# Kernel tuning notes

Measured on AMD Instinct MI355X. Metric: run time of the kernel, lower is better.

Reference implementation:

```python
import jax, jax.numpy as jnp
import numpy as np

N = 20000      # num nodes
E = 200000     # num edges (no self loops; GATConv adds them)
ND = 128       # node_feature_dim
ED = 64        # edge_feature_dim
H = 256        # hidden_dim (= GAT out_channels per head, concat=False)
HEADS = 4
L = 3          # num_gnn_layers


def setup_inputs() -> dict:
    key = jax.random.key(0)
    ks = jax.random.split(key, 24)
    rng = np.random.default_rng(0)
    src = rng.integers(0, N, size=E)
    dst = (src + 1 + rng.integers(0, N - 1, size=E)) % N  # guaranteed no self loops
    edge_index = jnp.asarray(np.stack([src, dst]), dtype=jnp.int32)
    s = 0.05
    inp = {
        'node_features': jax.random.normal(ks[0], (N, ND), jnp.float32),
        'edge_attr': jax.random.normal(ks[1], (E, ED), jnp.float32),
        'enc_w': jax.random.normal(ks[2], (ND, H), jnp.float32) * s,
        'enc_b': jnp.zeros((H,), jnp.float32),
        'edge_enc_w': jax.random.normal(ks[3], (L, ED, H), jnp.float32) * s,
        'edge_enc_b': jnp.zeros((L, H), jnp.float32),
        'gat_w': jax.random.normal(ks[4], (L, H, HEADS * H), jnp.float32) * s,
        'att_src': jax.random.normal(ks[5], (L, HEADS, H), jnp.float32) * s,
        'att_dst': jax.random.normal(ks[6], (L, HEADS, H), jnp.float32) * s,
        'att_edge': jax.random.normal(ks[7], (L, HEADS, H), jnp.float32) * s,
        'lin_edge_w': jax.random.normal(ks[8], (L, 1, HEADS * H), jnp.float32) * s,
        'gat_b': jnp.zeros((L, H), jnp.float32),
        'ln_g': jnp.ones((L, H), jnp.float32),
        'ln_b': jnp.zeros((L, H), jnp.float32),
        'head_w1': jax.random.normal(ks[9], (4, H, H // 2), jnp.float32) * s,
        'head_b1': jnp.zeros((4, H // 2), jnp.float32),
        'head_w2': jax.random.normal(ks[10], (4, H // 2, 1), jnp.float32) * s,
        'head_b2': jnp.zeros((4, 1), jnp.float32),
        'edge_index': edge_index,
    }
    return inp


def _layernorm(x, g, b, eps=1e-5):
    mu = x.mean(-1, keepdims=True)
    v = ((x - mu) ** 2).mean(-1, keepdims=True)
    return g * (x - mu) / jnp.sqrt(v + eps) + b


def _gat_layer(x, src, dst, ew_full, w, a_s_vec, a_d_vec, a_e_vec, lew, bias):
    # x: [N,H]; GATConv(heads=4, concat=False) with scalar edge feature (edge_dim=1)
    xp = (x @ w).reshape(N, HEADS, H)                       # [N,HEADS,H]
    a_s = (xp * a_s_vec).sum(-1)                            # [N,HEADS]
    a_d = (xp * a_d_vec).sum(-1)                            # [N,HEADS]
    ef = (ew_full[:, None] @ lew).reshape(-1, HEADS, H)     # [Etot,HEADS,H]
    a_e = (ef * a_e_vec).sum(-1)                            # [Etot,HEADS]
    logits = jax.nn.leaky_relu(a_s[src] + a_d[dst] + a_e, 0.2)
    m = jax.ops.segment_max(logits, dst, num_segments=N)    # segment softmax over dst
    p = jnp.exp(logits - m[dst])
    ssum = jax.ops.segment_sum(p, dst, num_segments=N)
    alpha = p / ssum[dst]                                   # [Etot,HEADS]
    out = jax.ops.segment_sum(alpha[:, :, None] * xp[src], dst, num_segments=N)
    return out.mean(1) + bias                               # concat=False -> mean over heads


def reference(node_features, edge_attr, enc_w, enc_b, edge_enc_w, edge_enc_b,
              gat_w, att_src, att_dst, att_edge, lin_edge_w, gat_b,
              ln_g, ln_b, head_w1, head_b1, head_w2, head_b2, edge_index):
    src0, dst0 = edge_index[0], edge_index[1]
    loop = jnp.arange(N, dtype=edge_index.dtype)
    src = jnp.concatenate([src0, loop])   # self loops appended (GATConv add_self_loops)
    dst = jnp.concatenate([dst0, loop])
    deg = jax.ops.segment_sum(jnp.ones((E,), node_features.dtype), dst0, num_segments=N)

    x = jax.nn.relu(node_features @ enc_w + enc_b)          # node encoder (dropout: eval)
    for l in range(L):
        ew = (edge_attr @ edge_enc_w[l] + edge_enc_b[l]).mean(-1)  # [E] scalar edge weight
        loop_w = jax.ops.segment_sum(ew, dst0, num_segments=N) / jnp.maximum(deg, 1.0)
        ew_full = jnp.concatenate([ew, loop_w])             # fill_value='mean' for self loops
        h = _gat_layer(x, src, dst, ew_full, gat_w[l], att_src[l], att_dst[l],
                       att_edge[l], lin_edge_w[l], gat_b[l])
        h = _layernorm(h, ln_g[l], ln_b[l])
        x = jax.nn.relu(x + h)
    emb = x                                                 # [N,H]

    # 4 prediction heads vectorized: k in {attrition, engagement, collaboration, anomaly}
    hmid = jax.nn.relu(jnp.einsum('nd,kdh->knh', emb, head_w1) + head_b1[:, None, :])
    o = jnp.einsum('knh,kho->kno', hmid, head_w2) + head_b2[:, None, :]  # [4,N,1]
    attrition = jax.nn.sigmoid(o[0])
    engagement = o[1]
    collaboration = o[2]
    anomaly = jax.nn.sigmoid(o[3])
    return (attrition, engagement, collaboration, anomaly, emb)
```

## Files before the change

kernel.cpp:

```cpp
#include <hip/hip_runtime.h>
#include <math.h>

#define N_NODES 20000
#define N_EDGES 200000
#define NDIM 128
#define EDIM 64
#define HDIM 256
#define HEADS 4
#define NH 1024
#define NLAYERS 3
#define SCAN_NBLK ((N_NODES + 255) / 256)

typedef __attribute__((ext_vector_type(8))) short short8;
typedef __attribute__((ext_vector_type(4))) float floatx4;

__device__ __forceinline__ float b2f(unsigned short u) {
    union { unsigned u; float f; } c; c.u = ((unsigned)u) << 16; return c.f;
}
__device__ __forceinline__ float b2f_lo(unsigned u) {
    union { unsigned u; float f; } c; c.u = u << 16; return c.f;
}
__device__ __forceinline__ float b2f_hi(unsigned u) {
    union { unsigned u; float f; } c; c.u = u & 0xffff0000u; return c.f;
}
__device__ __forceinline__ unsigned short f2b(float f) {
    union { float f; unsigned u; } c; c.f = f;
    unsigned u = c.u;
    return (unsigned short)((u + 0x7FFFu + ((u >> 16) & 1u)) >> 16);
}
__device__ __forceinline__ float lrelu(float v) { return v > 0.f ? v : 0.2f * v; }

__global__ void hist_kernel(const int* __restrict__ dst0, int* __restrict__ cnt) {
    int e = blockIdx.x * 256 + threadIdx.x;
    if (e < N_EDGES) atomicAdd(&cnt[dst0[e]], 1);
}

__global__ void scan_local(const int* __restrict__ cnt, int* __restrict__ row_ptr,
                           int* __restrict__ bsum) {
    __shared__ int wsum[4];
    int tid = threadIdx.x, lane = tid & 63, wid = tid >> 6;
    int n = blockIdx.x * 256 + tid;
    int v = (n < N_NODES) ? cnt[n] : 0;
    int s = v;
    #pragma unroll
    for (int off = 1; off < 64; off <<= 1) {
        int t = __shfl_up(s, off, 64);
        if (lane >= off) s += t;
    }
    if (lane == 63) wsum[wid] = s;
    __syncthreads();
    int woff = 0;
    #pragma unroll
    for (int w = 0; w < 4; w++) if (w < wid) woff += wsum[w];
    if (n < N_NODES) row_ptr[n] = woff + s - v;
    if (tid == 255) bsum[blockIdx.x] = woff + s;
}

__global__ void scan_bsums(int* __restrict__ bsum, int* __restrict__ boff) {
    __shared__ int wsum[2];
    int tid = threadIdx.x, lane = tid & 63, wid = tid >> 6;
    int v = (tid < SCAN_NBLK) ? bsum[tid] : 0;
    int s = v;
    #pragma unroll
    for (int off = 1; off < 64; off <<= 1) {
        int t = __shfl_up(s, off, 64);
        if (lane >= off) s += t;
    }
    if (lane == 63) wsum[wid] = s;
    __syncthreads();
    int woff = (wid == 1) ? wsum[0] : 0;
    if (tid < SCAN_NBLK) boff[tid] = woff + s - v;
    if (tid == SCAN_NBLK - 1) boff[SCAN_NBLK] = woff + s;
}

__global__ void scan_add(int* __restrict__ row_ptr, const int* __restrict__ boff) {
    int n = blockIdx.x * 256 + threadIdx.x;
    if (n < N_NODES) row_ptr[n] += boff[blockIdx.x];
    if (n == 0) row_ptr[N_NODES] = boff[SCAN_NBLK];
}

__global__ __launch_bounds__(256) void fill_ew(const int* __restrict__ src0,
                                               const int* __restrict__ dst0,
                                               const float* __restrict__ edge_attr,
                                               const float* __restrict__ wmean3,
                                               const float* __restrict__ scal3,
                                               const int* __restrict__ row_ptr,
                                               int* __restrict__ fillc,
                                               int* __restrict__ srcCSR,
                                               float* __restrict__ ewCSR4) {
    int e = blockIdx.x * 256 + threadIdx.x;
    if (e >= N_EDGES) return;
    int d = dst0[e];
    int p = atomicAdd(&fillc[d], 1);
    int pos = row_ptr[d] + p;
    srcCSR[pos] = src0[e];
    const float* row = edge_attr + (size_t)e * EDIM;
    float s0 = 0.f, s1 = 0.f, s2 = 0.f;
    #pragma unroll
    for (int dd = 0; dd < EDIM; dd += 4) {
        float4 a  = *(const float4*)(row + dd);
        float4 w0 = *(const float4*)(wmean3 + dd);
        float4 w1 = *(const float4*)(wmean3 + 64 + dd);
        float4 w2 = *(const float4*)(wmean3 + 128 + dd);
        s0 += a.x * w0.x + a.y * w0.y + a.z * w0.z + a.w * w0.w;
        s1 += a.x * w1.x + a.y * w1.y + a.z * w1.z + a.w * w1.w;
        s2 += a.x * w2.x + a.y * w2.y + a.z * w2.z + a.w * w2.w;
    }
    *(float4*)(ewCSR4 + (size_t)pos * 4) =
        make_float4(s0 + scal3[4], s1 + scal3[12], s2 + scal3[20], 0.f);
}

__global__ void transpose_bf(const float* __restrict__ in, unsigned short* __restrict__ out,
                             int K, int Nn, size_t in_bs, size_t out_bs) {
    in += blockIdx.z * in_bs;
    out += blockIdx.z * out_bs;
    __shared__ float sh[32][33];
    int tx = threadIdx.x, ty = threadIdx.y;
    int kb = blockIdx.y * 32, nb = blockIdx.x * 32;
    #pragma unroll
    for (int i = 0; i < 32; i += 8)
        sh[ty + i][tx] = in[(size_t)(kb + ty + i) * Nn + nb + tx];
    __syncthreads();
    #pragma unroll
    for (int i = 0; i < 32; i += 8)
        out[(size_t)(nb + ty + i) * K + kb + tx] = f2b(sh[tx][ty + i]);
}

__global__ void gat_w_prep(const float* __restrict__ in, unsigned short* __restrict__ out) {
    int z = blockIdx.z, l = z >> 2, h = z & 3;
    __shared__ float sh[32][33];
    int tx = threadIdx.x, ty = threadIdx.y;
    int kb = blockIdx.y * 32, db = blockIdx.x * 32;
    const float* src = in + (size_t)l * HDIM * NH + (size_t)h * HDIM;
    unsigned short* dst = out + (size_t)l * HDIM * NH + (size_t)h * HDIM;
    #pragma unroll
    for (int i = 0; i < 32; i += 8)
        sh[ty + i][tx] = src[(size_t)(kb + ty + i) * NH + db + tx];
    __syncthreads();
    #pragma unroll
    for (int i = 0; i < 32; i += 8)
        dst[(size_t)(db + ty + i) * NH + kb + tx] = f2b(0.25f * sh[tx][ty + i]);
}

__global__ void ws_prep(const float* __restrict__ gat_w, const float* __restrict__ att_src,
                        const float* __restrict__ att_dst,
                        float* __restrict__ ws_s, float* __restrict__ ws_d) {
    int l = blockIdx.x >> 2, h = blockIdx.x & 3;
    int k = threadIdx.x;
    const float* wrow = gat_w + (size_t)l * HDIM * NH + (size_t)k * NH + h * HDIM;
    const float* as = att_src + (size_t)l * NH + h * HDIM;
    const float* ad = att_dst + (size_t)l * NH + h * HDIM;
    float s1 = 0.f, s2 = 0.f;
    for (int d = 0; d < HDIM; d += 4) {
        float4 w4 = *(const float4*)(wrow + d);
        float4 a4 = *(const float4*)(as + d);
        float4 b4 = *(const float4*)(ad + d);
        s1 += w4.x * a4.x + w4.y * a4.y + w4.z * a4.z + w4.w * a4.w;
        s2 += w4.x * b4.x + w4.y * b4.y + w4.z * b4.z + w4.w * b4.w;
    }
    ws_s[(size_t)blockIdx.x * HDIM + k] = s1;
    ws_d[(size_t)blockIdx.x * HDIM + k] = s2;
}

__global__ void conv_bf(const float* __restrict__ in, unsigned short* __restrict__ out) {
    int i = blockIdx.x * 256 + threadIdx.x;
    float4 v = ((const float4*)in)[i];
    ushort4 o;
    o.x = f2b(v.x); o.y = f2b(v.y); o.z = f2b(v.z); o.w = f2b(v.w);
    ((ushort4*)out)[i] = o;
}

template <bool RELU, bool BIAS, bool HEAD2>
__global__ __launch_bounds__(256) void gemm_bf16(
    const unsigned short* __restrict__ A, const unsigned short* __restrict__ Bt,
    const float* __restrict__ bias, unsigned short* __restrict__ C,
    int M, int Ntot, int K,
    const float* __restrict__ w2 = nullptr, const float* __restrict__ b2v = nullptr,
    float* __restrict__ outp = nullptr)
{
    __shared__ char lds[16384];
    unsigned short* As = (unsigned short*)lds;
    unsigned short* Bs = (unsigned short*)(lds + 4096);
    unsigned short* Cs = (unsigned short*)lds;

    int Cb = Ntot >> 7;
    int P  = (M + 63) >> 6;
    int d  = blockIdx.x;
    int xcd = d & 7;
    int i5  = d >> 3;
    int p   = xcd + 8 * (i5 / Cb);
    int cblk = i5 % Cb;
    if (p >= P) return;
    int row0 = p * 64;
    int col0 = cblk * 128;

    int tid = threadIdx.x;
    int lane = tid & 63;
    int wid = tid >> 6;
    int wm = (wid >> 1) * 32;
    int wn = (wid & 1) * 64;
    int lm = lane & 15;
    int q8 = (lane >> 4) * 8;
    int q4 = (lane >> 4) * 4;

    floatx4 acc[2][4];
    #pragma unroll
    for (int i = 0; i < 2; i++)
        #pragma unroll
        for (int j = 0; j < 4; j++)
            acc[i][j] = (floatx4)(0.f);

    for (int k0 = 0; k0 < K; k0 += 32) {
        {
            int arow = tid >> 2;
            int acol = (tid & 3) * 8;
            int garow = row0 + arow; if (garow > M - 1) garow = M - 1;
            __builtin_amdgcn_global_load_lds(
                (__attribute__((address_space(1))) const void*)(A + (size_t)garow * K + k0 + acol),
                (__attribute__((address_space(3))) void*)(As + tid * 8), 16, 0, 0);
        }
        #pragma unroll
        for (int r = 0; r < 2; r++) {
            int chunk = tid + r * 256;
            int brow = chunk >> 2;
            int bcol = (chunk & 3) * 8;
            __builtin_amdgcn_global_load_lds(
                (__attribute__((address_space(1))) const void*)(Bt + (size_t)(col0 + brow) * K + k0 + bcol),
                (__attribute__((address_space(3))) void*)(Bs + chunk * 8), 16, 0, 0);
        }
        __syncthreads();
        short8 af[2], bf[4];
        #pragma unroll
        for (int i = 0; i < 2; i++)
            af[i] = *(const short8*)(As + (wm + i * 16 + lm) * 32 + q8);
        #pragma unroll
        for (int j = 0; j < 4; j++)
            bf[j] = *(const short8*)(Bs + (wn + j * 16 + lm) * 32 + q8);
        #pragma unroll
        for (int i = 0; i < 2; i++)
            #pragma unroll
            for (int j = 0; j < 4; j++)
                acc[i][j] = __builtin_amdgcn_mfma_f32_16x16x32_bf16(af[i], bf[j], acc[i][j], 0, 0, 0);
        __syncthreads();
    }

    #pragma unroll
    for (int i = 0; i < 2; i++) {
        #pragma unroll
        for (int j = 0; j < 4; j++) {
            int cl = wn + j * 16 + lm;
            float bv = BIAS ? bias[col0 + cl] : 0.f;
            #pragma unroll
            for (int reg = 0; reg < 4; reg++) {
                int rl = wm + i * 16 + q4 + reg;
                float v = acc[i][j][reg];
                if (BIAS) v += bv;
                if (RELU) v = fmaxf(v, 0.f);
                Cs[rl * 128 + cl] = f2b(v);
            }
        }
    }
    __syncthreads();
    if constexpr (!HEAD2) {
        int row = tid >> 2;
        int seg = (tid & 3) * 32;
        if (row0 + row < M) {
            #pragma unroll
            for (int u = 0; u < 4; u++) {
                int4 v = *(const int4*)(Cs + row * 128 + seg + u * 8);
                *(int4*)(C + (size_t)(row0 + row) * Ntot + col0 + seg + u * 8) = v;
            }
        }
    } else {
        int row = tid >> 2;
        int seg = (tid & 3) * 32;
        int k = col0 >> 7;
        const float* wr = w2 + k * 128;
        const unsigned short* cr = Cs + row * 128 + seg;
        float s = 0.f;
        #pragma unroll
        for (int u = 0; u < 4; u++) {
            int4 v = *(const int4*)(cr + u * 8);
            float4 w0 = *(const float4*)(wr + seg + u * 8);
            float4 w1 = *(const float4*)(wr + seg + u * 8 + 4);
            s += b2f_lo((unsigned)v.x) * w0.x + b2f_hi((unsigned)v.x) * w0.y
               + b2f_lo((unsigned)v.y) * w0.z + b2f_hi((unsigned)v.y) * w0.w;
            s += b2f_lo((unsigned)v.z) * w1.x + b2f_hi((unsigned)v.z) * w1.y
               + b2f_lo((unsigned)v.w) * w1.z + b2f_hi((unsigned)v.w) * w1.w;
        }
        s += __shfl_xor(s, 1, 64);
        s += __shfl_xor(s, 2, 64);
        if ((tid & 3) == 0 && row0 + row < M) {
            s += b2v[k];
            if (k == 0 || k == 3) s = 1.f / (1.f + __expf(-s));
            outp[(size_t)k * N_NODES + row0 + row] = s;
        }
    }
}

__global__ void layer_prep3(const float* __restrict__ edge_enc_w, const float* __restrict__ edge_enc_b,
                            const float* __restrict__ lin_edge_w, const float* __restrict__ att_edge,
                            float* __restrict__ wmean3, float* __restrict__ scal3)
{
    int l = blockIdx.x;
    const float* eew = edge_enc_w + (size_t)l * EDIM * HDIM;
    const float* eeb = edge_enc_b + (size_t)l * HDIM;
    const float* lew = lin_edge_w + (size_t)l * NH;
    const float* ae  = att_edge + (size_t)l * NH;
    float* wm = wmean3 + l * 64;
    float* sc = scal3 + l * 8;
    int tid = threadIdx.x;
    if (tid < 64) {
        float s = 0.f;
        for (int d = 0; d < HDIM; d++) s += eew[tid * HDIM + d];
        wm[tid] = s * (1.f / HDIM);
    } else if (tid < 68) {
        int h = tid - 64;
        float s = 0.f;
        for (int d = 0; d < HDIM; d++) s += lew[h * HDIM + d] * ae[h * HDIM + d];
        sc[h] = s;
    } else if (tid == 68) {
        float s = 0.f;
        for (int d = 0; d < HDIM; d++) s += eeb[d];
        sc[4] = s * (1.f / HDIM);
    }
}

__global__ void loop_weights_all(const float* __restrict__ ewCSR4, const int* __restrict__ row_ptr,
                                 float* __restrict__ loopw3)
{
    int n = blockIdx.x * 256 + threadIdx.x;
    if (n >= N_NODES) return;
    int r0 = row_ptr[n], r1 = row_ptr[n + 1];
    float s0 = 0.f, s1 = 0.f, s2 = 0.f;
    for (int i = r0; i < r1; i++) {
        float4 w = *(const float4*)(ewCSR4 + (size_t)i * 4);
        s0 += w.x; s1 += w.y; s2 += w.z;
    }
    float inv = 1.f / fmaxf((float)(r1 - r0), 1.f);
    loopw3[n] = s0 * inv;
    loopw3[N_NODES + n] = s1 * inv;
    loopw3[2 * N_NODES + n] = s2 * inv;
}

__global__ __launch_bounds__(256) void attn_x(const unsigned short* __restrict__ x_bf,
                                              const float* __restrict__ ws_s,
                                              const float* __restrict__ ws_d,
                                              float* __restrict__ a_s,
                                              float* __restrict__ a_d)
{
    int wid = threadIdx.x >> 6, lane = threadIdx.x & 63;
    int n = blockIdx.x * 4 + wid;
    ushort4 xv = *(const ushort4*)(x_bf + (size_t)n * HDIM + lane * 4);
    float x0 = b2f(xv.x), x1 = b2f(xv.y), x2 = b2f(xv.z), x3 = b2f(xv.w);
    float ss[4], sd[4];
    #pragma unroll
    for (int h = 0; h < 4; h++) {
        float4 s4 = *(const float4*)(ws_s + h * HDIM + lane * 4);
        float4 d4 = *(const float4*)(ws_d + h * HDIM + lane * 4);
        ss[h] = x0 * s4.x + x1 * s4.y + x2 * s4.z + x3 * s4.w;
        sd[h] = x0 * d4.x + x1 * d4.y + x2 * d4.z + x3 * d4.w;
    }
    #pragma unroll
    for (int off = 32; off > 0; off >>= 1)
        #pragma unroll
        for (int h = 0; h < 4; h++) {
            ss[h] += __shfl_xor(ss[h], off, 64);
            sd[h] += __shfl_xor(sd[h], off, 64);
        }
    if (lane == 0) {
        *(float4*)(a_s + n * 4) = make_float4(ss[0], ss[1], ss[2], ss[3]);
        *(float4*)(a_d + n * 4) = make_float4(sd[0], sd[1], sd[2], sd[3]);
    }
}

__global__ __launch_bounds__(256) void gat_agg_fused(
    const unsigned short* __restrict__ x_bf, const float* __restrict__ a_s,
    const float* __restrict__ a_d, const float* __restrict__ loopw,
    const float* __restrict__ scal, const int* __restrict__ row_ptr,
    const int* __restrict__ srcCSR, const float* __restrict__ ewCSR4,
    int l, unsigned short* __restrict__ agg)
{
    int wid = threadIdx.x >> 6, lane = threadIdx.x & 63;
    int n = blockIdx.x * 4 + wid;
    int r0 = row_ptr[n];
    int deg = row_ptr[n + 1] - r0;
    int cnt = deg + 1;

    float4 c4 = *(const float4*)scal;
    float4 as4 = *(const float4*)(a_s + (size_t)n * 4);
    float4 ad4 = *(const float4*)(a_d + (size_t)n * 4);
    float lw = loopw[n];
    float4 zself;
    zself.x = lrelu(as4.x + ad4.x + c4.x * lw);
    zself.y = lrelu(as4.y + ad4.y + c4.y * lw);
    zself.z = lrelu(as4.z + ad4.z + c4.z * lw);
    zself.w = lrelu(as4.w + ad4.w + c4.w * lw);

    auto comp_z = [&](int c0, int& sv, float4& z) {
        int ix = c0 + lane;
        if (ix < deg) {
            sv = srcCSR[r0 + ix];
            float w = ewCSR4[(((size_t)(r0 + ix)) << 2) + l];
            float4 zs = *(const float4*)(a_s + (size_t)sv * 4);
            z.x = lrelu(zs.x + ad4.x + c4.x * w);
            z.y = lrelu(zs.y + ad4.y + c4.y * w);
            z.z = lrelu(zs.z + ad4.z + c4.z * w);
            z.w = lrelu(zs.w + ad4.w + c4.w * w);
        } else if (ix == deg) {
            sv = n; z = zself;
        } else {
            sv = n; z.x = z.y = z.z = z.w = -1e30f;
        }
    };

    int sv0; float4 z0;
    comp_z(0, sv0, z0);
    float4 p0;
    p0.x = __expf(z0.x); p0.y = __expf(z0.y);
    p0.z = __expf(z0.z); p0.w = __expf(z0.w);
    float s0 = p0.x, s1 = p0.y, s2 = p0.z, s3 = p0.w;
    for (int c0 = 64; c0 < cnt; c0 += 64) {
        int sv; float4 z; comp_z(c0, sv, z);
        s0 += __expf(z.x); s1 += __expf(z.y);
        s2 += __expf(z.z); s3 += __expf(z.w);
    }
    #pragma unroll
    for (int off = 32; off > 0; off >>= 1) {
        s0 += __shfl_xor(s0, off, 64);
        s1 += __shfl_xor(s1, off, 64);
        s2 += __shfl_xor(s2, off, 64);
        s3 += __shfl_xor(s3, off, 64);
    }
    float i0 = 1.f / s0, i1 = 1.f / s1, i2 = 1.f / s2, i3 = 1.f / s3;
    float4 al0;
    al0.x = p0.x * i0; al0.y = p0.y * i1; al0.z = p0.z * i2; al0.w = p0.w * i3;

    float acc[4][4] = {};
    const unsigned short* xw = x_bf + (size_t)lane * 4;

    auto acc_one = [&](uint2 u, float a0, float a1, float a2, float a3) {
        float x0 = b2f_lo(u.x), x1 = b2f_hi(u.x), x2 = b2f_lo(u.y), x3 = b2f_hi(u.y);
        acc[0][0] += a0 * x0; acc[0][1] += a0 * x1; acc[0][2] += a0 * x2; acc[0][3] += a0 * x3;
        acc[1][0] += a1 * x0; acc[1][1] += a1 * x1; acc[1][2] += a1 * x2; acc[1][3] += a1 * x3;
        acc[2][0] += a2 * x0; acc[2][1] += a2 * x1; acc[2][2] += a2 * x2; acc[2][3] += a2 * x3;
        acc[3][0] += a3 * x0; acc[3][1] += a3 * x1; acc[3][2] += a3 * x2; acc[3][3] += a3 * x3;
    };

    auto agg_chunk = [&](int sv, float4 al, int mc) {
        int j = 0;
        for (; j + 3 < mc; j += 4) {
            int sA = __builtin_amdgcn_readfirstlane(__shfl(sv, j, 64));
            int sB = __builtin_amdgcn_readfirstlane(__shfl(sv, j + 1, 64));
            int sC = __builtin_amdgcn_readfirstlane(__shfl(sv, j + 2, 64));
            int sD = __builtin_amdgcn_readfirstlane(__shfl(sv, j + 3, 64));
            uint2 uA = *(const uint2*)(xw + (size_t)sA * HDIM);
            uint2 uB = *(const uint2*)(xw + (size_t)sB * HDIM);
            uint2 uC = *(const uint2*)(xw + (size_t)sC * HDIM);
            uint2 uD = *(const uint2*)(xw + (size_t)sD * HDIM);
            acc_one(uA, __shfl(al.x, j, 64), __shfl(al.y, j, 64),
                        __shfl(al.z, j, 64), __shfl(al.w, j, 64));
            acc_one(uB, __shfl(al.x, j + 1, 64), __shfl(al.y, j + 1, 64),
                        __shfl(al.z, j + 1, 64), __shfl(al.w, j + 1, 64));
            acc_one(uC, __shfl(al.x, j + 2, 64), __shfl(al.y, j + 2, 64),
                        __shfl(al.z, j + 2, 64), __shfl(al.w, j + 2, 64));
            acc_one(uD, __shfl(al.x, j + 3, 64), __shfl(al.y, j + 3, 64),
                        __shfl(al.z, j + 3, 64), __shfl(al.w, j + 3, 64));
        }
        for (; j + 1 < mc; j += 2) {
            int sA = __builtin_amdgcn_readfirstlane(__shfl(sv, j, 64));
            int sB = __builtin_amdgcn_readfirstlane(__shfl(sv, j + 1, 64));
            uint2 uA = *(const uint2*)(xw + (size_t)sA * HDIM);
            uint2 uB = *(const uint2*)(xw + (size_t)sB * HDIM);
            acc_one(uA, __shfl(al.x, j, 64), __shfl(al.y, j, 64),
                        __shfl(al.z, j, 64), __shfl(al.w, j, 64));
            acc_one(uB, __shfl(al.x, j + 1, 64), __shfl(al.y, j + 1, 64),
                        __shfl(al.z, j + 1, 64), __shfl(al.w, j + 1, 64));
        }
        if (j < mc) {
            int sA = __builtin_amdgcn_readfirstlane(__shfl(sv, j, 64));
            uint2 uA = *(const uint2*)(xw + (size_t)sA * HDIM);
            acc_one(uA, __shfl(al.x, j, 64), __shfl(al.y, j, 64),
                        __shfl(al.z, j, 64), __shfl(al.w, j, 64));
        }
    };

    agg_chunk(sv0, al0, min(64, cnt));
    for (int c0 = 64; c0 < cnt; c0 += 64) {
        int sv; float4 z; comp_z(c0, sv, z);
        float4 al;
        al.x = __expf(z.x) * i0; al.y = __expf(z.y) * i1;
        al.z = __expf(z.z) * i2; al.w = __expf(z.w) * i3;
        agg_chunk(sv, al, min(64, cnt - c0));
    }

    unsigned short* ag = agg + (size_t)n * NH + lane * 4;
    #pragma unroll
    for (int h = 0; h < 4; h++) {
        ushort4 o;
        o.x = f2b(acc[h][0]); o.y = f2b(acc[h][1]);
// ... 24 lines not shown
        s1 += __shfl_xor(s1, off, 64);
        s2 += __shfl_xor(s2, off, 64);
    }
    float mu = s1 * (1.f / HDIM);
    float var = s2 * (1.f / HDIM) - mu * mu;
    float rsig = rsqrtf(var + 1e-5f);
    float4 g = *(const float4*)(ln_g + lane * 4);
    float4 b = *(const float4*)(ln_b + lane * 4);
    ushort4 xv = *(const ushort4*)(x_bf + (size_t)n * HDIM + lane * 4);
    ushort4 o;
    o.x = f2b(fmaxf(b2f(xv.x) + g.x * (y0 - mu) * rsig + b.x, 0.f));
    o.y = f2b(fmaxf(b2f(xv.y) + g.y * (y1 - mu) * rsig + b.y, 0.f));
    o.z = f2b(fmaxf(b2f(xv.z) + g.z * (y2 - mu) * rsig + b.z, 0.f));
    o.w = f2b(fmaxf(b2f(xv.w) + g.w * (y3 - mu) * rsig + b.w, 0.f));
    *(ushort4*)(x_bf + (size_t)n * HDIM + lane * 4) = o;

    float xn0 = b2f(o.x), xn1 = b2f(o.y), xn2 = b2f(o.z), xn3 = b2f(o.w);
    if (EMB) {
        *(float4*)(emb_out + (size_t)n * HDIM + lane * 4) = make_float4(xn0, xn1, xn2, xn3);
    }
    if (ATTN) {
        float ss[4], sd[4];
        #pragma unroll
        for (int h = 0; h < 4; h++) {
            float4 s4 = *(const float4*)(ws_s + h * HDIM + lane * 4);
            float4 d4 = *(const float4*)(ws_d + h * HDIM + lane * 4);
            ss[h] = xn0 * s4.x + xn1 * s4.y + xn2 * s4.z + xn3 * s4.w;
            sd[h] = xn0 * d4.x + xn1 * d4.y + xn2 * d4.z + xn3 * d4.w;
        }
        #pragma unroll
        for (int off = 32; off > 0; off >>= 1)
            #pragma unroll
            for (int h = 0; h < 4; h++) {
                ss[h] += __shfl_xor(ss[h], off, 64);
                sd[h] += __shfl_xor(sd[h], off, 64);
            }
        if (lane == 0) {
            *(float4*)(a_s + n * 4) = make_float4(ss[0], ss[1], ss[2], ss[3]);
            *(float4*)(a_d + n * 4) = make_float4(sd[0], sd[1], sd[2], sd[3]);
        }
    }
}

extern "C" void kernel_launch(void* const* d_in, const int* in_sizes, int n_in,
                              void* d_out, int out_size, void* d_ws, size_t ws_size,
                              hipStream_t stream) {
    const float* node_features = (const float*)d_in[0];
    const float* edge_attr     = (const float*)d_in[1];
    const float* enc_w         = (const float*)d_in[2];
    const float* enc_b         = (const float*)d_in[3];
    const float* edge_enc_w    = (const float*)d_in[4];
    const float* edge_enc_b    = (const float*)d_in[5];
    const float* gat_w         = (const float*)d_in[6];
    const float* att_src       = (const float*)d_in[7];
    const float* att_dst       = (const float*)d_in[8];
    const float* att_edge      = (const float*)d_in[9];
    const float* lin_edge_w    = (const float*)d_in[10];
    const float* gat_b         = (const float*)d_in[11];
    const float* ln_g          = (const float*)d_in[12];
    const float* ln_b          = (const float*)d_in[13];
    const float* head_w1       = (const float*)d_in[14];
    const float* head_b1       = (const float*)d_in[15];
    const float* head_w2       = (const float*)d_in[16];
    const float* head_b2       = (const float*)d_in[17];
    const int*   edge_index    = (const int*)d_in[18];
    const int* src0 = edge_index;
    const int* dst0 = edge_index + N_EDGES;
    float* out = (float*)d_out;

    char* cur = (char*)d_ws;
    auto alloc = [&](size_t bytes) { char* p = cur; cur += (bytes + 255) & ~(size_t)255; return p; };
    unsigned short* x_bf   = (unsigned short*)alloc((size_t)N_NODES * HDIM * 2);
    unsigned short* agg    = (unsigned short*)alloc((size_t)N_NODES * NH * 2);
    unsigned short* y_bf   = (unsigned short*)alloc((size_t)N_NODES * HDIM * 2);
    unsigned short* nf_bf  = (unsigned short*)alloc((size_t)N_NODES * NDIM * 2);
    unsigned short* enc_wt = (unsigned short*)alloc((size_t)HDIM * NDIM * 2);
    unsigned short* gw2t   = (unsigned short*)alloc((size_t)NLAYERS * NH * HDIM * 2);
    unsigned short* hw1t   = (unsigned short*)alloc((size_t)512 * HDIM * 2);
    float* ws_s   = (float*)alloc((size_t)NLAYERS * 4 * HDIM * 4);
    float* ws_d   = (float*)alloc((size_t)NLAYERS * 4 * HDIM * 4);
    float* a_s    = (float*)alloc((size_t)N_NODES * 4 * 4);
    float* a_d    = (float*)alloc((size_t)N_NODES * 4 * 4);
    float* ewCSR4 = (float*)alloc((size_t)N_EDGES * 4 * 4);
    float* loopw3 = (float*)alloc((size_t)3 * N_NODES * 4);
    float* wmean3 = (float*)alloc(192 * 4);
    float* scal3  = (float*)alloc(24 * 4);
    int* cnt      = (int*)alloc((size_t)2 * N_NODES * 4);
    int* fillc    = cnt + N_NODES;
    int* row_ptr  = (int*)alloc((size_t)(N_NODES + 1) * 4);
    int* bsum     = (int*)alloc((size_t)(SCAN_NBLK + 1) * 4);
    int* boff     = (int*)alloc((size_t)(SCAN_NBLK + 1) * 4);
    int* srcCSR   = (int*)alloc((size_t)N_EDGES * 4);

    hipMemsetAsync(cnt, 0, (size_t)2 * N_NODES * sizeof(int), stream);

    layer_prep3<<<3, 128, 0, stream>>>(edge_enc_w, edge_enc_b, lin_edge_w, att_edge, wmean3, scal3);
    hist_kernel<<<(N_EDGES + 255) / 256, 256, 0, stream>>>(dst0, cnt);
    scan_local<<<SCAN_NBLK, 256, 0, stream>>>(cnt, row_ptr, bsum);
    scan_bsums<<<1, 128, 0, stream>>>(bsum, boff);
    scan_add<<<SCAN_NBLK, 256, 0, stream>>>(row_ptr, boff);
    fill_ew<<<(N_EDGES + 255) / 256, 256, 0, stream>>>(src0, dst0, edge_attr, wmean3, scal3,
                                                       row_ptr, fillc, srcCSR, ewCSR4);
    loop_weights_all<<<(N_NODES + 255) / 256, 256, 0, stream>>>(ewCSR4, row_ptr, loopw3);

    conv_bf<<<(N_NODES * NDIM / 4) / 256, 256, 0, stream>>>(node_features, nf_bf);
    transpose_bf<<<dim3(HDIM / 32, NDIM / 32, 1), dim3(32, 8), 0, stream>>>(
        enc_w, enc_wt, NDIM, HDIM, 0, 0);
    gat_w_prep<<<dim3(8, 8, 12), dim3(32, 8), 0, stream>>>(gat_w, gw2t);
    ws_prep<<<12, 256, 0, stream>>>(gat_w, att_src, att_dst, ws_s, ws_d);
    transpose_bf<<<dim3(128 / 32, HDIM / 32, 4), dim3(32, 8), 0, stream>>>(
        head_w1, hw1t, HDIM, 128, (size_t)HDIM * 128, (size_t)128 * HDIM);

    const int GEMM_GRID_256 = 8 * (((N_NODES + 63) / 64 + 7) / 8) * (256 / 128);
    const int GEMM_GRID_512 = 8 * (((N_NODES + 63) / 64 + 7) / 8) * (512 / 128);

    gemm_bf16<true, true, false><<<GEMM_GRID_256, 256, 0, stream>>>(
        nf_bf, enc_wt, enc_b, x_bf, N_NODES, HDIM, NDIM);
    attn_x<<<N_NODES / 4, 256, 0, stream>>>(x_bf, ws_s, ws_d, a_s, a_d);

    for (int l = 0; l < NLAYERS; l++) {
        gat_agg_fused<<<N_NODES / 4, 256, 0, stream>>>(
            x_bf, a_s, a_d, loopw3 + (size_t)l * N_NODES, scal3 + l * 8,
            row_ptr, srcCSR, ewCSR4, l, agg);
        gemm_bf16<false, true, false><<<GEMM_GRID_256, 256, 0, stream>>>(
            agg, gw2t + (size_t)l * NH * HDIM, gat_b + (size_t)l * HDIM, y_bf,
            N_NODES, HDIM, NH);
        if (l < NLAYERS - 1) {
            ln_residual<true, false><<<N_NODES / 4, 256, 0, stream>>>(
                y_bf, ln_g + (size_t)l * HDIM, ln_b + (size_t)l * HDIM, x_bf,
                ws_s + (size_t)(l + 1) * 4 * HDIM, ws_d + (size_t)(l + 1) * 4 * HDIM,
                a_s, a_d, nullptr);
        } else {
            ln_residual<false, true><<<N_NODES / 4, 256, 0, stream>>>(
                y_bf, ln_g + (size_t)l * HDIM, ln_b + (size_t)l * HDIM, x_bf,
                nullptr, nullptr, nullptr, nullptr, out + 4 * N_NODES);
        }
    }

    gemm_bf16<true, true, true><<<GEMM_GRID_512, 256, 0, stream>>>(
        x_bf, hw1t, head_b1, nullptr, N_NODES, 512, HDIM,
        head_w2, head_b2, out);
}
```

Measured before the change: 427.0 us.

## Merge prep kernels, single-block scan, fold loop weights into aggregation, deepen GEMM K-step

Several small preprocessing launches (bf16 conversion, weight transposes, ws_prep, layer_prep) are merged into one multi-role kernel, and the three-kernel scan becomes a single 1024-thread block. The loop_weights_all kernel is removed; each aggregation wave now computes its self-loop mean edge weight by a wave reduction over its CSR row. The GEMM processes K in 64-wide steps with double-size LDS tiles to halve barrier count, and the head GEMM is split into its own kernel. These cut launch overhead and sync, at the cost of a serial one-block scan and a slightly higher LDS footprint.

```diff
diff --git a/kernel.cpp b/kernel.cpp
--- a/kernel.cpp
+++ b/kernel.cpp
@@ -9,7 +9,6 @@
 #define HEADS 4
 #define NH 1024
 #define NLAYERS 3
-#define SCAN_NBLK ((N_NODES + 255) / 256)
 
 typedef __attribute__((ext_vector_type(8))) short short8;
 typedef __attribute__((ext_vector_type(4))) float floatx4;
@@ -35,48 +34,38 @@
     if (e < N_EDGES) atomicAdd(&cnt[dst0[e]], 1);
 }
 
-__global__ void scan_local(const int* __restrict__ cnt, int* __restrict__ row_ptr,
-                           int* __restrict__ bsum) {
-    __shared__ int wsum[4];
-    int tid = threadIdx.x, lane = tid & 63, wid = tid >> 6;
-    int n = blockIdx.x * 256 + tid;
-    int v = (n < N_NODES) ? cnt[n] : 0;
-    int s = v;
+__global__ __launch_bounds__(1024) void scan_full(const int* __restrict__ cnt,
+                                                  int* __restrict__ row_ptr) {
+    const int PER = 20;
+    __shared__ int wtot[16];
+    int t = threadIdx.x, lane = t & 63, wid = t >> 6;
+    int base = t * PER;
+    int loc[PER];
+    int s = 0;
+    #pragma unroll
+    for (int i = 0; i < PER; i++) {
+        int idx = base + i;
+        int v = (idx < N_NODES) ? cnt[idx] : 0;
+        loc[i] = s; s += v;
+    }
+    int inc = s;
     #pragma unroll
     for (int off = 1; off < 64; off <<= 1) {
-        int t = __shfl_up(s, off, 64);
-        if (lane >= off) s += t;
-    }
-    if (lane == 63) wsum[wid] = s;
+        int tt = __shfl_up(inc, off, 64);
+        if (lane >= off) inc += tt;
+    }
+    if (lane == 63) wtot[wid] = inc;
     __syncthreads();
     int woff = 0;
     #pragma unroll
-    for (int w = 0; w < 4; w++) if (w < wid) woff += wsum[w];
-    if (n < N_NODES) row_ptr[n] = woff + s - v;
-    if (tid == 255) bsum[blockIdx.x] = woff + s;
-}
-
-__global__ void scan_bsums(int* __restrict__ bsum, int* __restrict__ boff) {
-    __shared__ int wsum[2];
-    int tid = threadIdx.x, lane = tid & 63, wid = tid >> 6;
-    int v = (tid < SCAN_NBLK) ? bsum[tid] : 0;
-    int s = v;
-    #pragma unroll
-    for (int off = 1; off < 64; off <<= 1) {
-        int t = __shfl_up(s, off, 64);
-        if (lane >= off) s += t;
-    }
-    if (lane == 63) wsum[wid] = s;
-    __syncthreads();
-    int woff = (wid == 1) ? wsum[0] : 0;
-    if (tid < SCAN_NBLK) boff[tid] = woff + s - v;
-    if (tid == SCAN_NBLK - 1) boff[SCAN_NBLK] = woff + s;
-}
-
-__global__ void scan_add(int* __restrict__ row_ptr, const int* __restrict__ boff) {
-    int n = blockIdx.x * 256 + threadIdx.x;
-    if (n < N_NODES) row_ptr[n] += boff[blockIdx.x];
-    if (n == 0) row_ptr[N_NODES] = boff[SCAN_NBLK];
+    for (int w = 0; w < 16; w++) if (w < wid) woff += wtot[w];
+    int excl = woff + inc - s;
+    #pragma unroll
+    for (int i = 0; i < PER; i++) {
+        int idx = base + i;
+        if (idx < N_NODES) row_ptr[idx] = excl + loc[i];
+    }
+    if (t == 1023) row_ptr[N_NODES] = excl + s;
 }
 
 __global__ __launch_bounds__(256) void fill_ew(const int* __restrict__ src0,
@@ -110,77 +99,121 @@
         make_float4(s0 + scal3[4], s1 + scal3[12], s2 + scal3[20], 0.f);
 }
 
-__global__ void transpose_bf(const float* __restrict__ in, unsigned short* __restrict__ out,
-                             int K, int Nn, size_t in_bs, size_t out_bs) {
-    in += blockIdx.z * in_bs;
-    out += blockIdx.z * out_bs;
-    __shared__ float sh[32][33];
-    int tx = threadIdx.x, ty = threadIdx.y;
-    int kb = blockIdx.y * 32, nb = blockIdx.x * 32;
+#define PC_CONV   2500
+#define PC_TENC   (PC_CONV + 32)
+#define PC_GWP    (PC_TENC + 768)
+#define PC_WSP    (PC_GWP + 12)
+#define PC_THW1   (PC_WSP + 128)
+#define PC_TOTAL  (PC_THW1 + 3)
+
+__device__ void transpose_body(const float* in, unsigned short* out, int K, int Nn,
+                               int bx, int by, float sh[32][33], float scale) {
+    int tid = threadIdx.x;
+    int tx = tid & 31, ty = tid >> 5;
+    int kb = by * 32, nb = bx * 32;
     #pragma unroll
     for (int i = 0; i < 32; i += 8)
         sh[ty + i][tx] = in[(size_t)(kb + ty + i) * Nn + nb + tx];
     __syncthreads();
     #pragma unroll
     for (int i = 0; i < 32; i += 8)
-        out[(size_t)(nb + ty + i) * K + kb + tx] = f2b(sh[tx][ty + i]);
-}
-
-__global__ void gat_w_prep(const float* __restrict__ in, unsigned short* __restrict__ out) {
-    int z = blockIdx.z, l = z >> 2, h = z & 3;
+        out[(size_t)(nb + ty + i) * K + kb + tx] = f2b(scale * sh[tx][ty + i]);
+}
+
+__global__ __launch_bounds__(256) void prep_combo(
+    const float* __restrict__ node_features, unsigned short* __restrict__ nf_bf,
+    const float* __restrict__ enc_w, unsigned short* __restrict__ enc_wt,
+    const float* __restrict__ gat_w, unsigned short* __restrict__ gw2t,
+    const float* __restrict__ att_src, const float* __restrict__ att_dst,
+    float* __restrict__ ws_s, float* __restrict__ ws_d,
+    const float* __restrict__ head_w1, unsigned short* __restrict__ hw1t,
+    const float* __restrict__ edge_enc_w, const float* __restrict__ edge_enc_b,
+    const float* __restrict__ lin_edge_w, const float* __restrict__ att_edge,
+    float* __restrict__ wmean3, float* __restrict__ scal3)
+{
     __shared__ float sh[32][33];
-    int tx = threadIdx.x, ty = threadIdx.y;
-    int kb = blockIdx.y * 32, db = blockIdx.x * 32;
-    const float* src = in + (size_t)l * HDIM * NH + (size_t)h * HDIM;
-    unsigned short* dst = out + (size_t)l * HDIM * NH + (size_t)h * HDIM;
-    #pragma unroll
-    for (int i = 0; i < 32; i += 8)
-        sh[ty + i][tx] = src[(size_t)(kb + ty + i) * NH + db + tx];
-    __syncthreads();
-    #pragma unroll
-    for (int i = 0; i < 32; i += 8)
-        dst[(size_t)(db + ty + i) * NH + kb + tx] = f2b(0.25f * sh[tx][ty + i]);
-}
-
-__global__ void ws_prep(const float* __restrict__ gat_w, const float* __restrict__ att_src,
-                        const float* __restrict__ att_dst,
-                        float* __restrict__ ws_s, float* __restrict__ ws_d) {
-    int l = blockIdx.x >> 2, h = blockIdx.x & 3;
-    int k = threadIdx.x;
-    const float* wrow = gat_w + (size_t)l * HDIM * NH + (size_t)k * NH + h * HDIM;
-    const float* as = att_src + (size_t)l * NH + h * HDIM;
-    const float* ad = att_dst + (size_t)l * NH + h * HDIM;
-    float s1 = 0.f, s2 = 0.f;
-    for (int d = 0; d < HDIM; d += 4) {
-        float4 w4 = *(const float4*)(wrow + d);
-        float4 a4 = *(const float4*)(as + d);
-        float4 b4 = *(const float4*)(ad + d);
-        s1 += w4.x * a4.x + w4.y * a4.y + w4.z * a4.z + w4.w * a4.w;
-        s2 += w4.x * b4.x + w4.y * b4.y + w4.z * b4.z + w4.w * b4.w;
-    }
-    ws_s[(size_t)blockIdx.x * HDIM + k] = s1;
-    ws_d[(size_t)blockIdx.x * HDIM + k] = s2;
-}
-
-__global__ void conv_bf(const float* __restrict__ in, unsigned short* __restrict__ out) {
-    int i = blockIdx.x * 256 + threadIdx.x;
-    float4 v = ((const float4*)in)[i];
-    ushort4 o;
-    o.x = f2b(v.x); o.y = f2b(v.y); o.z = f2b(v.z); o.w = f2b(v.w);
-    ((ushort4*)out)[i] = o;
-}
-
-template <bool RELU, bool BIAS, bool HEAD2>
+    int b = blockIdx.x;
+    int tid = threadIdx.x;
+    if (b < PC_CONV) {
+        int i = b * 256 + tid;
+        float4 v = ((const float4*)node_features)[i];
+        ushort4 o;
+        o.x = f2b(v.x); o.y = f2b(v.y); o.z = f2b(v.z); o.w = f2b(v.w);
+        ((ushort4*)nf_bf)[i] = o;
+    } else if (b < PC_TENC) {
+        int b2 = b - PC_CONV;
+        transpose_body(enc_w, enc_wt, NDIM, HDIM, b2 & 7, b2 >> 3, sh, 1.f);
+    } else if (b < PC_GWP) {
+        int b3 = b - PC_TENC;
+        int bx = b3 & 7, by = (b3 >> 3) & 7, z = b3 >> 6;
+        int l = z >> 2, h = z & 3;
+        const float* src = gat_w + (size_t)l * HDIM * NH + (size_t)h * HDIM;
+        unsigned short* dst = gw2t + (size_t)l * HDIM * NH + (size_t)h * HDIM;
+        int tx = tid & 31, ty = tid >> 5;
+        int kb = by * 32, db = bx * 32;
+        #pragma unroll
+        for (int i = 0; i < 32; i += 8)
+            sh[ty + i][tx] = src[(size_t)(kb + ty + i) * NH + db + tx];
+        __syncthreads();
+        #pragma unroll
+        for (int i = 0; i < 32; i += 8)
+            dst[(size_t)(db + ty + i) * NH + kb + tx] = f2b(0.25f * sh[tx][ty + i]);
+    } else if (b < PC_WSP) {
+        int bx = b - PC_GWP;
+        int l = bx >> 2, h = bx & 3;
+        int k = tid;
+        const float* wrow = gat_w + (size_t)l * HDIM * NH + (size_t)k * NH + h * HDIM;
+        const float* as = att_src + (size_t)l * NH + h * HDIM;
+        const float* ad = att_dst + (size_t)l * NH + h * HDIM;
+        float s1 = 0.f, s2 = 0.f;
+        for (int d = 0; d < HDIM; d += 4) {
+            float4 w4 = *(const float4*)(wrow + d);
+            float4 a4 = *(const float4*)(as + d);
+            float4 b4 = *(const float4*)(ad + d);
+            s1 += w4.x * a4.x + w4.y * a4.y + w4.z * a4.z + w4.w * a4.w;
+            s2 += w4.x * b4.x + w4.y * b4.y + w4.z * b4.z + w4.w * b4.w;
+        }
+        ws_s[(size_t)bx * HDIM + k] = s1;
+        ws_d[(size_t)bx * HDIM + k] = s2;
+    } else if (b < PC_THW1) {
+        int b4 = b - PC_WSP;
+        int bx = b4 & 3, by = (b4 >> 2) & 7, z = b4 >> 5;
+        transpose_body(head_w1 + (size_t)z * HDIM * 128,
+                       hw1t + (size_t)z * 128 * HDIM, HDIM, 128, bx, by, sh, 1.f);
+    } else {
+        int l = b - PC_THW1;
+        const float* eew = edge_enc_w + (size_t)l * EDIM * HDIM;
+        const float* eeb = edge_enc_b + (size_t)l * HDIM;
+        const float* lew = lin_edge_w + (size_t)l * NH;
+        const float* ae  = att_edge + (size_t)l * NH;
+        float* wm = wmean3 + l * 64;
+        float* sc = scal3 + l * 8;
+        if (tid < 64) {
+            float s = 0.f;
+            for (int d = 0; d < HDIM; d++) s += eew[tid * HDIM + d];
+            wm[tid] = s * (1.f / HDIM);
+        } else if (tid < 68) {
+            int h = tid - 64;
+            float s = 0.f;
+            for (int d = 0; d < HDIM; d++) s += lew[h * HDIM + d] * ae[h * HDIM + d];
+            sc[h] = s;
+        } else if (tid == 68) {
+            float s = 0.f;
+            for (int d = 0; d < HDIM; d++) s += eeb[d];
+            sc[4] = s * (1.f / HDIM);
+        }
+    }
+}
+
+template <bool RELU, bool BIAS>
 __global__ __launch_bounds__(256) void gemm_bf16(
     const unsigned short* __restrict__ A, const unsigned short* __restrict__ Bt,
     const float* __restrict__ bias, unsigned short* __restrict__ C,
-    int M, int Ntot, int K,
-    const float* __restrict__ w2 = nullptr, const float* __restrict__ b2v = nullptr,
-    float* __restrict__ outp = nullptr)
+    int M, int Ntot, int K)
 {
-    __shared__ char lds[16384];
+    __shared__ char lds[24576];
     unsigned short* As = (unsigned short*)lds;
-    unsigned short* Bs = (unsigned short*)(lds + 4096);
+    unsigned short* Bs = (unsigned short*)(lds + 8192);
     unsigned short* Cs = (unsigned short*)lds;
 
     int Cb = Ntot >> 7;
@@ -210,37 +243,43 @@
         for (int j = 0; j < 4; j++)
             acc[i][j] = (floatx4)(0.f);
 
-    for (int k0 = 0; k0 < K; k0 += 32) {
-        {
-            int arow = tid >> 2;
-            int acol = (tid & 3) * 8;
-            int garow = row0 + arow; if (garow > M - 1) garow = M - 1;
+    int arow = tid >> 2;
+    int acol = (tid & 3) * 8;
+    int garow = row0 + arow; if (garow > M - 1) garow = M - 1;
+
+    for (int k0 = 0; k0 < K; k0 += 64) {
+        #pragma unroll
+        for (int kk = 0; kk < 2; kk++) {
+            int kb = k0 + kk * 32;
             __builtin_amdgcn_global_load_lds(
-                (__attribute__((address_space(1))) const void*)(A + (size_t)garow * K + k0 + acol),
-                (__attribute__((address_space(3))) void*)(As + tid * 8), 16, 0, 0);
-        }
-        #pragma unroll
-        for (int r = 0; r < 2; r++) {
-            int chunk = tid + r * 256;
-            int brow = chunk >> 2;
-            int bcol = (chunk & 3) * 8;
-            __builtin_amdgcn_global_load_lds(
-                (__attribute__((address_space(1))) const void*)(Bt + (size_t)(col0 + brow) * K + k0 + bcol),
-                (__attribute__((address_space(3))) void*)(Bs + chunk * 8), 16, 0, 0);
+                (__attribute__((address_space(1))) const void*)(A + (size_t)garow * K + kb + acol),
+                (__attribute__((address_space(3))) void*)(As + kk * 2048 + tid * 8), 16, 0, 0);
+            #pragma unroll
+            for (int r = 0; r < 2; r++) {
+                int chunk = tid + r * 256;
+                int brow = chunk >> 2;
+                int bcol = (chunk & 3) * 8;
+                __builtin_amdgcn_global_load_lds(
+                    (__attribute__((address_space(1))) const void*)(Bt + (size_t)(col0 + brow) * K + kb + bcol),
+                    (__attribute__((address_space(3))) void*)(Bs + kk * 4096 + chunk * 8), 16, 0, 0);
+            }
         }
         __syncthreads();
-        short8 af[2], bf[4];
-        #pragma unroll
-        for (int i = 0; i < 2; i++)
-            af[i] = *(const short8*)(As + (wm + i * 16 + lm) * 32 + q8);
-        #pragma unroll
-        for (int j = 0; j < 4; j++)
-            bf[j] = *(const short8*)(Bs + (wn + j * 16 + lm) * 32 + q8);
-        #pragma unroll
-        for (int i = 0; i < 2; i++)
+        #pragma unroll
+        for (int kk = 0; kk < 2; kk++) {
+            short8 af[2], bf[4];
+            #pragma unroll
+            for (int i = 0; i < 2; i++)
+                af[i] = *(const short8*)(As + kk * 2048 + (wm + i * 16 + lm) * 32 + q8);
             #pragma unroll
             for (int j = 0; j < 4; j++)
-                acc[i][j] = __builtin_amdgcn_mfma_f32_16x16x32_bf16(af[i], bf[j], acc[i][j], 0, 0, 0);
+                bf[j] = *(const short8*)(Bs + kk * 4096 + (wn + j * 16 + lm) * 32 + q8);
+            #pragma unroll
+            for (int i = 0; i < 2; i++)
+                #pragma unroll
+                for (int j = 0; j < 4; j++)
+                    acc[i][j] = __builtin_amdgcn_mfma_f32_16x16x32_bf16(af[i], bf[j], acc[i][j], 0, 0, 0);
+        }
         __syncthreads();
     }
 
@@ -261,86 +300,133 @@
         }
     }
     __syncthreads();
-    if constexpr (!HEAD2) {
-        int row = tid >> 2;
-        int seg = (tid & 3) * 32;
-        if (row0 + row < M) {
-            #pragma unroll
-            for (int u = 0; u < 4; u++) {
-                int4 v = *(const int4*)(Cs + row * 128 + seg + u * 8);
-                *(int4*)(C + (size_t)(row0 + row) * Ntot + col0 + seg + u * 8) = v;
+    int row = tid >> 2;
+    int seg = (tid & 3) * 32;
+    if (row0 + row < M) {
+        #pragma unroll
+        for (int u = 0; u < 4; u++) {
+            int4 v = *(const int4*)(Cs + row * 128 + seg + u * 8);
+            *(int4*)(C + (size_t)(row0 + row) * Ntot + col0 + seg + u * 8) = v;
+        }
+    }
+}
+
+__global__ __launch_bounds__(256) void gemm_head(
+    const unsigned short* __restrict__ A, const unsigned short* __restrict__ Bt,
+    const float* __restrict__ bias, int M, int Ntot, int K,
+    const float* __restrict__ w2, const float* __restrict__ b2v,
+    float* __restrict__ outp)
+{
+    __shared__ char lds[24576];
+    unsigned short* As = (unsigned short*)lds;
+    unsigned short* Bs = (unsigned short*)(lds + 8192);
+    unsigned short* Cs = (unsigned short*)lds;
+
+    int Cb = Ntot >> 7;
+    int P  = (M + 63) >> 6;
+    int d  = blockIdx.x;
+    int xcd = d & 7;
+    int i5  = d >> 3;
+    int p   = xcd + 8 * (i5 / Cb);
+    int cblk = i5 % Cb;
+    if (p >= P) return;
+    int row0 = p * 64;
+    int col0 = cblk * 128;
+
+    int tid = threadIdx.x;
+    int lane = tid & 63;
+    int wid = tid >> 6;
+    int wm = (wid >> 1) * 32;
+    int wn = (wid & 1) * 64;
+    int lm = lane & 15;
+    int q8 = (lane >> 4) * 8;
+    int q4 = (lane >> 4) * 4;
+
+    floatx4 acc[2][4];
+    #pragma unroll
+    for (int i = 0; i < 2; i++)
+        #pragma unroll
+        for (int j = 0; j < 4; j++)
+            acc[i][j] = (floatx4)(0.f);
+
+    int arow = tid >> 2;
+    int acol = (tid & 3) * 8;
+    int garow = row0 + arow; if (garow > M - 1) garow = M - 1;
+
+    for (int k0 = 0; k0 < K; k0 += 64) {
+        #pragma unroll
+        for (int kk = 0; kk < 2; kk++) {
+            int kb = k0 + kk * 32;
+            __builtin_amdgcn_global_load_lds(
+                (__attribute__((address_space(1))) const void*)(A + (size_t)garow * K + kb + acol),
+                (__attribute__((address_space(3))) void*)(As + kk * 2048 + tid * 8), 16, 0, 0);
+            #pragma unroll
+            for (int r = 0; r < 2; r++) {
+                int chunk = tid + r * 256;
+                int brow = chunk >> 2;
+                int bcol = (chunk & 3) * 8;
+                __builtin_amdgcn_global_load_lds(
+                    (__attribute__((address_space(1))) const void*)(Bt + (size_t)(col0 + brow) * K + kb + bcol),
+                    (__attribute__((address_space(3))) void*)(Bs + kk * 4096 + chunk * 8), 16, 0, 0);
             }
         }
-    } else {
-        int row = tid >> 2;
-        int seg = (tid & 3) * 32;
-        int k = col0 >> 7;
-        const float* wr = w2 + k * 128;
-        const unsigned short* cr = Cs + row * 128 + seg;
-        float s = 0.f;
-        #pragma unroll
-        for (int u = 0; u < 4; u++) {
-            int4 v = *(const int4*)(cr + u * 8);
-            float4 w0 = *(const float4*)(wr + seg + u * 8);
-            float4 w1 = *(const float4*)(wr + seg + u * 8 + 4);
-            s += b2f_lo((unsigned)v.x) * w0.x + b2f_hi((unsigned)v.x) * w0.y
-               + b2f_lo((unsigned)v.y) * w0.z + b2f_hi((unsigned)v.y) * w0.w;
-            s += b2f_lo((unsigned)v.z) * w1.x + b2f_hi((unsigned)v.z) * w1.y
-               + b2f_lo((unsigned)v.w) * w1.z + b2f_hi((unsigned)v.w) * w1.w;
-        }
-        s += __shfl_xor(s, 1, 64);
-        s += __shfl_xor(s, 2, 64);
-        if ((tid & 3) == 0 && row0 + row < M) {
-            s += b2v[k];
-            if (k == 0 || k == 3) s = 1.f / (1.f + __expf(-s));
-            outp[(size_t)k * N_NODES + row0 + row] = s;
-        }
-    }
-}
-
-__global__ void layer_prep3(const float* __restrict__ edge_enc_w, const float* __restrict__ edge_enc_b,
-                            const float* __restrict__ lin_edge_w, const float* __restrict__ att_edge,
-                            float* __restrict__ wmean3, float* __restrict__ scal3)
-{
-    int l = blockIdx.x;
-    const float* eew = edge_enc_w + (size_t)l * EDIM * HDIM;
-    const float* eeb = edge_enc_b + (size_t)l * HDIM;
-    const float* lew = lin_edge_w + (size_t)l * NH;
-    const float* ae  = att_edge + (size_t)l * NH;
-    float* wm = wmean3 + l * 64;
-    float* sc = scal3 + l * 8;
-    int tid = threadIdx.x;
-    if (tid < 64) {
-        float s = 0.f;
-        for (int d = 0; d < HDIM; d++) s += eew[tid * HDIM + d];
-        wm[tid] = s * (1.f / HDIM);
-    } else if (tid < 68) {
-        int h = tid - 64;
-        float s = 0.f;
-        for (int d = 0; d < HDIM; d++) s += lew[h * HDIM + d] * ae[h * HDIM + d];
-        sc[h] = s;
-    } else if (tid == 68) {
-        float s = 0.f;
-        for (int d = 0; d < HDIM; d++) s += eeb[d];
-        sc[4] = s * (1.f / HDIM);
-    }
-}
-
-__global__ void loop_weights_all(const float* __restrict__ ewCSR4, const int* __restrict__ row_ptr,
-                                 float* __restrict__ loopw3)
-{
-    int n = blockIdx.x * 256 + threadIdx.x;
-    if (n >= N_NODES) return;
-    int r0 = row_ptr[n], r1 = row_ptr[n + 1];
-    float s0 = 0.f, s1 = 0.f, s2 = 0.f;
-    for (int i = r0; i < r1; i++) {
-        float4 w = *(const float4*)(ewCSR4 + (size_t)i * 4);
-        s0 += w.x; s1 += w.y; s2 += w.z;
-    }
-    float inv = 1.f / fmaxf((float)(r1 - r0), 1.f);
-    loopw3[n] = s0 * inv;
-    loopw3[N_NODES + n] = s1 * inv;
-    loopw3[2 * N_NODES + n] = s2 * inv;
+        __syncthreads();
+        #pragma unroll
+        for (int kk = 0; kk < 2; kk++) {
+            short8 af[2], bf[4];
+            #pragma unroll
+            for (int i = 0; i < 2; i++)
+                af[i] = *(const short8*)(As + kk * 2048 + (wm + i * 16 + lm) * 32 + q8);
+            #pragma unroll
+            for (int j = 0; j < 4; j++)
+                bf[j] = *(const short8*)(Bs + kk * 4096 + (wn + j * 16 + lm) * 32 + q8);
+            #pragma unroll
+            for (int i = 0; i < 2; i++)
+                #pragma unroll
+                for (int j = 0; j < 4; j++)
+                    acc[i][j] = __builtin_amdgcn_mfma_f32_16x16x32_bf16(af[i], bf[j], acc[i][j], 0, 0, 0);
+        }
+        __syncthreads();
+    }
+
+    #pragma unroll
+    for (int i = 0; i < 2; i++) {
+        #pragma unroll
+        for (int j = 0; j < 4; j++) {
+            int cl = wn + j * 16 + lm;
+            float bv = bias[col0 + cl];
+            #pragma unroll
+            for (int reg = 0; reg < 4; reg++) {
+                int rl = wm + i * 16 + q4 + reg;
+                float v = fmaxf(acc[i][j][reg] + bv, 0.f);
+                Cs[rl * 128 + cl] = f2b(v);
+            }
+        }
+    }
+    __syncthreads();
+    int row = tid >> 2;
+    int seg = (tid & 3) * 32;
+    int k = col0 >> 7;
+    const float* wr = w2 + k * 128;
+    const unsigned short* cr = Cs + row * 128 + seg;
+    float s = 0.f;
+    #pragma unroll
+    for (int u = 0; u < 4; u++) {
+        int4 v = *(const int4*)(cr + u * 8);
+        float4 w0 = *(const float4*)(wr + seg + u * 8);
+        float4 w1 = *(const float4*)(wr + seg + u * 8 + 4);
+        s += b2f_lo((unsigned)v.x) * w0.x + b2f_hi((unsigned)v.x) * w0.y
+           + b2f_lo((unsigned)v.y) * w0.z + b2f_hi((unsigned)v.y) * w0.w;
+        s += b2f_lo((unsigned)v.z) * w1.x + b2f_hi((unsigned)v.z) * w1.y
+           + b2f_lo((unsigned)v.w) * w1.z + b2f_hi((unsigned)v.w) * w1.w;
+    }
+    s += __shfl_xor(s, 1, 64);
+    s += __shfl_xor(s, 2, 64);
+    if ((tid & 3) == 0 && row0 + row < M) {
+        s += b2v[k];
+        if (k == 0 || k == 3) s = 1.f / (1.f + __expf(-s));
+        outp[(size_t)k * N_NODES + row0 + row] = s;
+    }
 }
 
 __global__ __launch_bounds__(256) void attn_x(const unsigned short* __restrict__ x_bf,
@@ -376,7 +462,7 @@
 
 __global__ __launch_bounds__(256) void gat_agg_fused(
     const unsigned short* __restrict__ x_bf, const float* __restrict__ a_s,
-    const float* __restrict__ a_d, const float* __restrict__ loopw,
+    const float* __restrict__ a_d,
     const float* __restrict__ scal, const int* __restrict__ row_ptr,
     const int* __restrict__ srcCSR, const float* __restrict__ ewCSR4,
     int l, unsigned short* __restrict__ agg)
@@ -390,7 +476,21 @@
     float4 c4 = *(const float4*)scal;
     float4 as4 = *(const float4*)(a_s + (size_t)n * 4);
     float4 ad4 = *(const float4*)(a_d + (size_t)n * 4);
-    float lw = loopw[n];
+
+    int sv0 = n; float w0 = 0.f;
+    if (lane < deg) {
+        sv0 = srcCSR[r0 + lane];
+        w0 = ewCSR4[(((size_t)(r0 + lane)) << 2) + l];
+    }
+    float sw = w0;
+    for (int c0 = 64; c0 < deg; c0 += 64) {
+        int i2 = c0 + lane;
+        if (i2 < deg) sw += ewCSR4[(((size_t)(r0 + i2)) << 2) + l];
+    }
+    #pragma unroll
+    for (int off = 32; off > 0; off >>= 1) sw += __shfl_xor(sw, off, 64);
+    float lw = sw / fmaxf((float)deg, 1.f);
+
     float4 zself;
     zself.x = lrelu(as4.x + ad4.x + c4.x * lw);
     zself.y = lrelu(as4.y + ad4.y + c4.y * lw);
@@ -414,8 +514,19 @@
         }
     };
 
-    int sv0; float4 z0;
-    comp_z(0, sv0, z0);
+    float4 z0;
+    if (lane < deg) {
+        float4 zs = *(const float4*)(a_s + (size_t)sv0 * 4);
+        z0.x = lrelu(zs.x + ad4.x + c4.x * w0);
+        z0.y = lrelu(zs.y + ad4.y + c4.y * w0);
+        z0.z = lrelu(zs.z + ad4.z + c4.z * w0);
+        z0.w = lrelu(zs.w + ad4.w + c4.w * w0);
+    } else if (lane == deg) {
+        z0 = zself;
+    } else {
+        z0.x = z0.y = z0.z = z0.w = -1e30f;
+    }
+
     float4 p0;
     p0.x = __expf(z0.x); p0.y = __expf(z0.y);
     p0.z = __expf(z0.z); p0.w = __expf(z0.w);
@@ -606,47 +717,35 @@
     float* a_s    = (float*)alloc((size_t)N_NODES * 4 * 4);
     float* a_d    = (float*)alloc((size_t)N_NODES * 4 * 4);
     float* ewCSR4 = (float*)alloc((size_t)N_EDGES * 4 * 4);
-    float* loopw3 = (float*)alloc((size_t)3 * N_NODES * 4);
     float* wmean3 = (float*)alloc(192 * 4);
     float* scal3  = (float*)alloc(24 * 4);
     int* cnt      = (int*)alloc((size_t)2 * N_NODES * 4);
     int* fillc    = cnt + N_NODES;
     int* row_ptr  = (int*)alloc((size_t)(N_NODES + 1) * 4);
-    int* bsum     = (int*)alloc((size_t)(SCAN_NBLK + 1) * 4);
-    int* boff     = (int*)alloc((size_t)(SCAN_NBLK + 1) * 4);
     int* srcCSR   = (int*)alloc((size_t)N_EDGES * 4);
 
     hipMemsetAsync(cnt, 0, (size_t)2 * N_NODES * sizeof(int), stream);
 
-    layer_prep3<<<3, 128, 0, stream>>>(edge_enc_w, edge_enc_b, lin_edge_w, att_edge, wmean3, scal3);
+    prep_combo<<<PC_TOTAL, 256, 0, stream>>>(
+        node_features, nf_bf, enc_w, enc_wt, gat_w, gw2t, att_src, att_dst,
+        ws_s, ws_d, head_w1, hw1t, edge_enc_w, edge_enc_b, lin_edge_w, att_edge,
+        wmean3, scal3);
     hist_kernel<<<(N_EDGES + 255) / 256, 256, 0, stream>>>(dst0, cnt);
-    scan_local<<<SCAN_NBLK, 256, 0, stream>>>(cnt, row_ptr, bsum);
-    scan_bsums<<<1, 128, 0, stream>>>(bsum, boff);
-    scan_add<<<SCAN_NBLK, 256, 0, stream>>>(row_ptr, boff);
+    scan_full<<<1, 1024, 0, stream>>>(cnt, row_ptr);
     fill_ew<<<(N_EDGES + 255) / 256, 256, 0, stream>>>(src0, dst0, edge_attr, wmean3, scal3,
                                                        row_ptr, fillc, srcCSR, ewCSR4);
-    loop_weights_all<<<(N_NODES + 255) / 256, 256, 0, stream>>>(ewCSR4, row_ptr, loopw3);
-
-    conv_bf<<<(N_NODES * NDIM / 4) / 256, 256, 0, stream>>>(node_features, nf_bf);
-    transpose_bf<<<dim3(HDIM / 32, NDIM / 32, 1), dim3(32, 8), 0, stream>>>(
-        enc_w, enc_wt, NDIM, HDIM, 0, 0);
-    gat_w_prep<<<dim3(8, 8, 12), dim3(32, 8), 0, stream>>>(gat_w, gw2t);
-    ws_prep<<<12, 256, 0, stream>>>(gat_w, att_src, att_dst, ws_s, ws_d);
-    transpose_bf<<<dim3(128 / 32, HDIM / 32, 4), dim3(32, 8), 0, stream>>>(
-        head_w1, hw1t, HDIM, 128, (size_t)HDIM * 128, (size_t)128 * HDIM);
 
     const int GEMM_GRID_256 = 8 * (((N_NODES + 63) / 64 + 7) / 8) * (256 / 128);
-    const int GEMM_GRID_512 = 8 * (((N_NODES + 63) / 64 + 7) / 8) * (512 / 128);
-
-    gemm_bf16<true, true, false><<<GEMM_GRID_256, 256, 0, stream>>>(
+    const int GRID_HEAD = 8 * (((N_NODES + 63) / 64 + 7) / 8) * (512 / 128);
+
+    gemm_bf16<true, true><<<GEMM_GRID_256, 256, 0, stream>>>(
         nf_bf, enc_wt, enc_b, x_bf, N_NODES, HDIM, NDIM);
     attn_x<<<N_NODES / 4, 256, 0, stream>>>(x_bf, ws_s, ws_d, a_s, a_d);
 
     for (int l = 0; l < NLAYERS; l++) {
         gat_agg_fused<<<N_NODES / 4, 256, 0, stream>>>(
-            x_bf, a_s, a_d, loopw3 + (size_t)l * N_NODES, scal3 + l * 8,
-            row_ptr, srcCSR, ewCSR4, l, agg);
-        gemm_bf16<false, true, false><<<GEMM_GRID_256, 256, 0, stream>>>(
+            x_bf, a_s, a_d, scal3 + l * 8, row_ptr, srcCSR, ewCSR4, l, agg);
+        gemm_bf16<false, true><<<GEMM_GRID_256, 256, 0, stream>>>(
             agg, gw2t + (size_t)l * NH * HDIM, gat_b + (size_t)l * HDIM, y_bf,
             N_NODES, HDIM, NH);
         if (l < NLAYERS - 1) {
@@ -661,7 +760,6 @@
         }
     }
 
-    gemm_bf16<true, true, true><<<GEMM_GRID_512, 256, 0, stream>>>(
-        x_bf, hw1t, head_b1, nullptr, N_NODES, 512, HDIM,
-        head_w2, head_b2, out);
-}
+    gemm_head<<<GRID_HEAD, 256, 0, stream>>>(
+        x_bf, hw1t, head_b1, N_NODES, 512, HDIM, head_w2, head_b2, out);
+}
```

New measurement: 413.6 us. 3.1% less time.
